# Kernel optimization log

Hardware: AMD Instinct MI355X
Metric: run time of the kernel (lower is better)

Reference implementation:

```python
import jax, jax.numpy as jnp
import numpy as np

N_NODES = 20000
N_EDGES = 320000
N_GRAPHS = 32
IN_CH = 5
HID = 64
HEADS = 4
DH = HID // HEADS  # 16
LAYERS = 8
EPS = 1e-5
SLOPE = 0.2


def setup_inputs() -> dict:
    key = jax.random.key(0)
    ks = jax.random.split(key, 32)
    inp = {}
    inp['x1'] = jax.random.normal(ks[0], (N_NODES, IN_CH), dtype=jnp.float32)
    inp['x2'] = jax.random.normal(ks[1], (N_NODES, IN_CH), dtype=jnp.float32)
    inp['edge_index1'] = jax.random.randint(ks[2], (2, N_EDGES), 0, N_NODES, dtype=jnp.int32)
    inp['edge_index2'] = jax.random.randint(ks[3], (2, N_EDGES), 0, N_NODES, dtype=jnp.int32)
    inp['batch1'] = jnp.sort(jax.random.randint(ks[4], (N_NODES,), 0, N_GRAPHS, dtype=jnp.int32))
    inp['batch2'] = jnp.sort(jax.random.randint(ks[5], (N_NODES,), 0, N_GRAPHS, dtype=jnp.int32))
    # node_lin
    inp['Wn'] = jax.random.normal(ks[6], (IN_CH, HID), dtype=jnp.float32) / np.sqrt(IN_CH)
    inp['bnode'] = jnp.zeros((HID,), dtype=jnp.float32)
    # GATv2 layers (stacked over LAYERS)
    s = 1.0 / np.sqrt(HID)
    inp['Wl'] = jax.random.normal(ks[7], (LAYERS, HID, HID), dtype=jnp.float32) * s
    inp['bl'] = jnp.zeros((LAYERS, HID), dtype=jnp.float32)
    inp['Wr'] = jax.random.normal(ks[8], (LAYERS, HID, HID), dtype=jnp.float32) * s
    inp['br'] = jnp.zeros((LAYERS, HID), dtype=jnp.float32)
    inp['att'] = jax.random.normal(ks[9], (LAYERS, HEADS, DH), dtype=jnp.float32) / np.sqrt(DH)
    inp['cbias'] = jnp.zeros((LAYERS, HID), dtype=jnp.float32)
    # batch norms
    inp['gamma'] = jnp.ones((LAYERS, HID), dtype=jnp.float32)
    inp['beta'] = jnp.zeros((LAYERS, HID), dtype=jnp.float32)
    # fc head
    inp['f1w'] = jax.random.normal(ks[10], (2 * HID, 256), dtype=jnp.float32) / np.sqrt(2 * HID)
    inp['f1b'] = jnp.zeros((256,), dtype=jnp.float32)
    inp['f2w'] = jax.random.normal(ks[11], (256, 128), dtype=jnp.float32) / np.sqrt(256)
    inp['f2b'] = jnp.zeros((128,), dtype=jnp.float32)
    inp['f3w'] = jax.random.normal(ks[12], (128, 1), dtype=jnp.float32) / np.sqrt(128)
    inp['f3b'] = jnp.zeros((1,), dtype=jnp.float32)
    return inp


def _gatv2_layer(x, src, dst, Wl, bl, Wr, br, att, bias):
    # x: [N, HID]; src/dst: [E'] (self loops included)
    N = x.shape[0]
    xl = (x @ Wl + bl).reshape(N, HEADS, DH)  # source transform
    xr = (x @ Wr + br).reshape(N, HEADS, DH)  # target transform
    e = jax.nn.leaky_relu(xl[src] + xr[dst], SLOPE)          # [E, H, DH]
    score = jnp.einsum('ehd,hd->eh', e, att)                  # [E, H]
    smax = jax.ops.segment_max(score, dst, num_segments=N)    # [N, H]
    ex = jnp.exp(score - smax[dst])
    denom = jax.ops.segment_sum(ex, dst, num_segments=N)
    alpha = ex / denom[dst]                                   # [E, H]
    msg = alpha[:, :, None] * xl[src]                         # [E, H, DH]
    out = jax.ops.segment_sum(msg, dst, num_segments=N)       # [N, H, DH]
    return out.reshape(N, HID) + bias


def _forward_once(x, edge_index, batch, Wn, bnode, Wl, bl, Wr, br, att, cbias, gamma, beta):
    N = x.shape[0]
    loop = jnp.arange(N, dtype=edge_index.dtype)
    src = jnp.concatenate([edge_index[0], loop])  # add_self_loops=True
    dst = jnp.concatenate([edge_index[1], loop])
    h = x @ Wn + bnode
    for l in range(LAYERS):
        g = _gatv2_layer(h, src, dst, Wl[l], bl[l], Wr[l], br[l], att[l], cbias[l])
        mu = g.mean(axis=0)
        var = g.var(axis=0)
        g = (g - mu) / jnp.sqrt(var + EPS) * gamma[l] + beta[l]
        h = h + jax.nn.elu(g)
    # global_mean_pool
    sums = jax.ops.segment_sum(h, batch, num_segments=N_GRAPHS)
    cnt = jax.ops.segment_sum(jnp.ones((N,), dtype=h.dtype), batch, num_segments=N_GRAPHS)
    return sums / jnp.maximum(cnt, 1.0)[:, None]


def reference(x1, edge_index1, batch1, x2, edge_index2, batch2, Wn, bnode, Wl, bl, Wr, br, att, cbias, gamma, beta, f1w, f1b, f2w, f2b, f3w, f3b):
    o1 = _forward_once(x1, edge_index1, batch1, Wn, bnode, Wl, bl, Wr, br, att, cbias, gamma, beta)
    o2 = _forward_once(x2, edge_index2, batch2, Wn, bnode, Wl, bl, Wr, br, att, cbias, gamma, beta)
    c = jnp.concatenate([o1, o2], axis=1)           # [G, 128]
    h = jax.nn.relu(c @ f1w + f1b)                   # dropout = identity (eval)
    h = jax.nn.relu(h @ f2w + f2b)
    return h @ f3w + f3b                             # [G, 1]
```

## Files before the change

### kernel.cpp

```cpp
#include <hip/hip_runtime.h>
#include <hip/hip_bf16.h>

#define N_NODES 20000
#define HID 64
#define EPS 1e-5f

struct GP {
    const int* ei;
    const int* batch;
    const float* x;
    int* deg;
    int* cursor;
    int* csr;
    float* h;
    float* xl;
    float* xr;
    float* gb;
    float* stats;
    float* osum;
};


__global__ void k_csr_init(GP a, GP b, int n, int two) {
    int t = blockIdx.x * blockDim.x + threadIdx.x;
    if (t < n) {
        a.deg[t] = 1;
        if (two) b.deg[t] = 1;
    }
}

__global__ void k_count(GP a, GP b, int Ea, int Eb, int two) {
    int t = blockIdx.x * blockDim.x + threadIdx.x;
    if (t < Ea) atomicAdd(&a.deg[a.ei[Ea + t]], 1);
    if (two && t < Eb) atomicAdd(&b.deg[b.ei[Eb + t]], 1);
}

#define SCAN_T 1024
#define SCAN_C 20
__global__ __launch_bounds__(1024) void k_scan(GP a, GP b, int n, int totA, int totB) {
    GP g = blockIdx.x ? b : a;
    int total = blockIdx.x ? totB : totA;
    __shared__ int sd[SCAN_T];
    int t = threadIdx.x;
    int base = t * SCAN_C;
    int loc[SCAN_C];
    int s = 0;
#pragma unroll
    for (int i = 0; i < SCAN_C; ++i) {
        int idx = base + i;
        loc[i] = (idx < n) ? g.deg[idx] : 0;
        s += loc[i];
    }
    sd[t] = s;
    __syncthreads();
    for (int off = 1; off < SCAN_T; off <<= 1) {
        int v = (t >= off) ? sd[t - off] : 0;
        __syncthreads();
        sd[t] += v;
        __syncthreads();
    }
    int run = sd[t] - s;
#pragma unroll
    for (int i = 0; i < SCAN_C; ++i) {
        int idx = base + i;
        if (idx < n) { g.deg[idx] = run; g.cursor[idx] = run; run += loc[i]; }
    }
    if (t == 0) g.deg[n] = total;
}

__global__ void k_scatter(GP a, GP b, int Ea, int Eb, int n, int two) {
    int t = blockIdx.x * blockDim.x + threadIdx.x;
    if (t < Ea) {
        int s = a.ei[t], d = a.ei[Ea + t];
        a.csr[atomicAdd(&a.cursor[d], 1)] = s;
    } else if (t < Ea + n) {
        int nn = t - Ea;
        a.csr[atomicAdd(&a.cursor[nn], 1)] = nn;
    }
    if (two) {
        if (t < Eb) {
            int s = b.ei[t], d = b.ei[Eb + t];
            b.csr[atomicAdd(&b.cursor[d], 1)] = s;
        } else if (t < Eb + n) {
            int nn = t - Eb;
            b.csr[atomicAdd(&b.cursor[nn], 1)] = nn;
        }
    }
}


__global__ void k_nodelin(GP a, GP b, int nPer, const float* __restrict__ Wn,
                          const float* __restrict__ bn, int n) {
    int bid = blockIdx.x;
    GP g = a;
    if (bid >= nPer) { g = b; bid -= nPer; }
    int idx = bid * 256 + threadIdx.x;
    if (idx >= n * HID) return;
    int node = idx >> 6, c = idx & 63;
    float acc = bn[c];
#pragma unroll
    for (int k = 0; k < 5; ++k) acc += g.x[node * 5 + k] * Wn[k * HID + c];
    g.h[idx] = acc;
}


__global__ __launch_bounds__(256) void k_lin2(GP ga, GP gbp, int nPer, int n,
        const float* __restrict__ Wl, const float* __restrict__ bl,
        const float* __restrict__ Wr, const float* __restrict__ br,
        const float* __restrict__ gamma, const float* __restrict__ beta, int layer) {
    __shared__ float wls[4096], wrs[4096];
    __shared__ float hs[2048];
    int bid = blockIdx.x;
    GP g = ga;
    if (bid >= nPer) { g = gbp; bid -= nPer; }
    {
        const float4* wl4 = (const float4*)Wl;
        const float4* wr4 = (const float4*)Wr;
        float4* l4 = (float4*)wls;
        float4* r4 = (float4*)wrs;
        for (int i = threadIdx.x; i < 1024; i += 256) { l4[i] = wl4[i]; r4[i] = wr4[i]; }
    }
    int c = threadIdx.x & 63;
    int wid = threadIdx.x >> 6;
    float blv = bl[c], brv = br[c];
    float mu = 0.f, inv = 1.f, gam = 1.f, bet = 0.f;
    if (layer > 0) {
        const float* st = g.stats + (layer - 1) * 128;
        float invn = 1.0f / (float)n;
        mu = st[c] * invn;
        float var = st[64 + c] * invn - mu * mu;
        inv = rsqrtf(fmaxf(var, 0.f) + EPS);
        gam = gamma[c]; bet = beta[c];
    }
    __syncthreads();
    float* hw = &hs[wid * 512];
    const float4* hw4 = (const float4*)hw;
    for (int base = bid * 32; base < n; base += nPer * 32) {
        int nb = base + wid * 8;
        size_t off0 = (size_t)nb * 64 + c;
        float hv[8];
        if (layer > 0) {
#pragma unroll
            for (int j = 0; j < 8; ++j) {
                float gv = g.gb[off0 + j * 64];
                float ov = g.h[off0 + j * 64];
                float v = (gv - mu) * inv * gam + bet;
                v = v > 0.f ? v : expm1f(v);
                hv[j] = ov + v;
                g.h[off0 + j * 64] = hv[j];
            }
        } else {
#pragma unroll
            for (int j = 0; j < 8; ++j) hv[j] = g.h[off0 + j * 64];
        }
#pragma unroll
        for (int j = 0; j < 8; ++j) hw[j * 64 + c] = hv[j];
        float accl[8], accr[8];
#pragma unroll
        for (int j = 0; j < 8; ++j) { accl[j] = blv; accr[j] = brv; }
        for (int k4 = 0; k4 < 16; ++k4) {
            float4 hq[8];
#pragma unroll
            for (int j = 0; j < 8; ++j) hq[j] = hw4[j * 16 + k4];
#pragma unroll
            for (int kk = 0; kk < 4; ++kk) {
                float wl = wls[(k4 * 4 + kk) * 64 + c];
                float wr = wrs[(k4 * 4 + kk) * 64 + c];
#pragma unroll
                for (int j = 0; j < 8; ++j) {
                    float hx = (&hq[j].x)[kk];
                    accl[j] = fmaf(hx, wl, accl[j]);
                    accr[j] = fmaf(hx, wr, accr[j]);
                }
            }
        }
#pragma unroll
        for (int j = 0; j < 8; ++j) {
            g.xl[off0 + j * 64] = accl[j];
            g.xr[off0 + j * 64] = accr[j];
        }
    }
}


__device__ __forceinline__ float red16(float p) {
    p += __int_as_float(__builtin_amdgcn_update_dpp(0, __float_as_int(p), 0xB1, 0xF, 0xF, true));
    p += __int_as_float(__builtin_amdgcn_update_dpp(0, __float_as_int(p), 0x4E, 0xF, 0xF, true));
    p += __int_as_float(__builtin_amdgcn_update_dpp(0, __float_as_int(p), 0x141, 0xF, 0xF, true));
    p += __int_as_float(__builtin_amdgcn_update_dpp(0, __float_as_int(p), 0x140, 0xF, 0xF, true));
    return p;
}

__global__ __launch_bounds__(512) void k_attn(GP ga, GP gbp, int nPer,
        const float* __restrict__ att, const float* __restrict__ cbias, int layer, int n) {
    int bid = blockIdx.x;
    GP g = ga;
    if (bid >= nPer) { g = gbp; bid -= nPer; }
    int lane = threadIdx.x & 63;
    int wid = threadIdx.x >> 6;
    int gw = bid * 8 + wid;
    int nw = nPer * 8;
    float attv = att[lane];
    float attv2 = attv * 0.2f;
    float cb = cbias[lane];
    const int* __restrict__ rowptr = g.deg;
    const int* __restrict__ csr = g.csr;
    const float* __restrict__ xl = g.xl;
    const float* __restrict__ xr = g.xr;
    float* __restrict__ gbuf = g.gb;
    float* st = g.stats + layer * 128;
    float bsum = 0.f, bsq = 0.f;
    for (int node = gw; node < n; node += nw) {
        int start = rowptr[node], end = rowptr[node + 1];
        float xrv = xr[(size_t)node * 64 + lane];
        float ts = xl[(size_t)node * 64 + lane] + xrv;
        float sself = red16(ts * (ts > 0.f ? attv : attv2));
        float lsum = 0.f, acc = 0.f;
        int idx = start;
        for (; idx + 8 <= end; idx += 8) {
            int sidx[8];
            float xv[8];
#pragma unroll
            for (int j = 0; j < 8; ++j) sidx[j] = csr[idx + j];
#pragma unroll
            for (int j = 0; j < 8; ++j) xv[j] = xl[(size_t)sidx[j] * 64 + lane];
#pragma unroll
            for (int j = 0; j < 8; ++j) {
                float t = xv[j] + xrv;
                float p = red16(t * (t > 0.f ? attv : attv2));
                float w = __expf(fminf(p - sself, 80.f));
                lsum += w;
                acc = fmaf(w, xv[j], acc);
            }
        }
        for (; idx + 4 <= end; idx += 4) {
            int sidx[4];
            float xv[4];
#pragma unroll
            for (int j = 0; j < 4; ++j) sidx[j] = csr[idx + j];
#pragma unroll
            for (int j = 0; j < 4; ++j) xv[j] = xl[(size_t)sidx[j] * 64 + lane];
#pragma unroll
            for (int j = 0; j < 4; ++j) {
                float t = xv[j] + xrv;
                float p = red16(t * (t > 0.f ? attv : attv2));
                float w = __expf(fminf(p - sself, 80.f));
                lsum += w;
                acc = fmaf(w, xv[j], acc);
            }
        }
        for (; idx < end; ++idx) {
            int s0 = csr[idx];
            float x0 = xl[(size_t)s0 * 64 + lane];
            float t0 = x0 + xrv;
            float p0 = red16(t0 * (t0 > 0.f ? attv : attv2));
            float w0 = __expf(fminf(p0 - sself, 80.f));
            lsum += w0;
            acc = fmaf(w0, x0, acc);
        }
        float outv = acc / lsum + cb;
        gbuf[(size_t)node * 64 + lane] = outv;
        bsum += outv; bsq += outv * outv;
    }
    __shared__ float sred[512];
    sred[threadIdx.x] = bsum;
    __syncthreads();
    if (threadIdx.x < 64) {
        float t = 0.f;
#pragma unroll
        for (int w = 0; w < 8; ++w) t += sred[w * 64 + threadIdx.x];
        atomicAdd(&st[threadIdx.x], t);
    }
    __syncthreads();
    sred[threadIdx.x] = bsq;
    __syncthreads();
    if (threadIdx.x < 64) {
        float t = 0.f;
#pragma unroll
        for (int w = 0; w < 8; ++w) t += sred[w * 64 + threadIdx.x];
        atomicAdd(&st[64 + threadIdx.x], t);
    }
}


__global__ __launch_bounds__(256) void k_pool(GP ga, GP gbp, int nPer,
        const float* __restrict__ gamma, const float* __restrict__ beta, int n) {
    int bid = blockIdx.x;
    GP g = ga;
    if (bid >= nPer) { g = gbp; bid -= nPer; }
    int lane = threadIdx.x & 63, w = threadIdx.x >> 6;
    const float* st = g.stats + 7 * 128;
    float invn = 1.f / (float)n;
    float mu = st[lane] * invn;
    float var = st[64 + lane] * invn - mu * mu;
    float inv = rsqrtf(fmaxf(var, 0.f) + EPS);
    float gam = gamma[lane], bet = beta[lane];
    int chunk = (n + nPer - 1) / nPer;
    int s = bid * chunk;
    int e = min(s + chunk, n);
    float acc = 0.f;
    int cur = -1;
    for (int node = s + w; node < e; node += 4) {
        int bg = g.batch[node];
        size_t off = (size_t)node * 64 + lane;
        float gv = g.gb[off];
        float hv = g.h[off];
        float v = (gv - mu) * inv * gam + bet;
        float hn = hv + (v > 0.f ? v : expm1f(v));
        if (bg != cur) {
            if (cur >= 0) atomicAdd(&g.osum[cur * 64 + lane], acc);
            acc = 0.f; cur = bg;
        }
        acc += hn;
    }
    if (cur >= 0) atomicAdd(&g.osum[cur * 64 + lane], acc);
}


__device__ __forceinline__ int lb(const int* __restrict__ b, int n, int v) {
    int lo = 0, hi = n;
    while (lo < hi) { int mid = (lo + hi) >> 1; if (b[mid] < v) lo = mid + 1; else hi = mid; }
    return lo;
}

__global__ __launch_bounds__(256) void k_fc(const float* __restrict__ o1, const float* __restrict__ o2,
                                            const int* __restrict__ b1, const int* __restrict__ b2,
                                            const float* __restrict__ f1w, const float* __restrict__ f1b,
                                            const float* __restrict__ f2w, const float* __restrict__ f2b,
                                            const float* __restrict__ f3w, const float* __restrict__ f3b,
                                            float* __restrict__ out, int n) {
    int gid = blockIdx.x, t = threadIdx.x;
    __shared__ float cin[128];
    __shared__ float h1[256];
    __shared__ float red[128];
    __shared__ int cnts[2];
    if (t == 0) cnts[0] = lb(b1, n, gid + 1) - lb(b1, n, gid);
    if (t == 1) cnts[1] = lb(b2, n, gid + 1) - lb(b2, n, gid);
    __syncthreads();
    if (t < 64) {
        float c1 = (float)(cnts[0] > 0 ? cnts[0] : 1);
        float c2 = (float)(cnts[1] > 0 ? cnts[1] : 1);
        cin[t] = o1[gid * 64 + t] / c1;
        cin[64 + t] = o2[gid * 64 + t] / c2;
    }
    __syncthreads();
    float a = f1b[t];
#pragma unroll 8
    for (int k = 0; k < 128; ++k) a += cin[k] * f1w[k * 256 + t];
    h1[t] = fmaxf(a, 0.f);
    __syncthreads();
    if (t < 128) {
        float a2 = f2b[t];
#pragma unroll 8
        for (int k = 0; k < 256; ++k) a2 += h1[k] * f2w[k * 128 + t];
        red[t] = fmaxf(a2, 0.f) * f3w[t];
    }
    __syncthreads();
    for (int off = 64; off > 0; off >>= 1) {
        if (t < off) red[t] += red[t + off];
        __syncthreads();
    }
    if (t == 0) out[gid] = red[0] + f3b[0];
}


extern "C" void kernel_launch(void* const* d_in, const int* in_sizes, int n_in,
                              void* d_out, int out_size, void* d_ws, size_t ws_size,
                              hipStream_t stream) {
    const float* x1 = (const float*)d_in[0];
    const float* x2 = (const float*)d_in[1];
    const int* ei1 = (const int*)d_in[2];
    const int* ei2 = (const int*)d_in[3];
    const int* b1 = (const int*)d_in[4];
    const int* b2 = (const int*)d_in[5];
    const float* Wn = (const float*)d_in[6];
    const float* bnode = (const float*)d_in[7];
    const float* Wl = (const float*)d_in[8];
    const float* bl = (const float*)d_in[9];
    const float* Wr = (const float*)d_in[10];
    const float* br = (const float*)d_in[11];
    const float* att = (const float*)d_in[12];
    const float* cbias = (const float*)d_in[13];
    const float* gamma = (const float*)d_in[14];
    const float* beta = (const float*)d_in[15];
    const float* f1w = (const float*)d_in[16];
    const float* f1b = (const float*)d_in[17];
    const float* f2w = (const float*)d_in[18];
    const float* f2b = (const float*)d_in[19];
    const float* f3w = (const float*)d_in[20];
    const float* f3b = (const float*)d_in[21];
    float* out = (float*)d_out;

    const int N = N_NODES;
    const int EA = in_sizes[2] / 2;
    const int EB = in_sizes[3] / 2;
    const size_t INT_PG = 20096 + 20096 + 340096;
    const size_t BIG = (size_t)N * 64;
    const size_t SMALL = 2 * 1024 + 2 * 2048;
    const size_t dualBytes = 2 * INT_PG * 4 + (8 * BIG + SMALL) * 4;
    const int dual = (ws_size >= dualBytes) ? 1 : 0;

    int* ibase = (int*)d_ws;
    int* iA = ibase;
    int* iB = dual ? ibase + INT_PG : ibase;
    float* fbase = (float*)(ibase + (size_t)(dual ? 2 : 1) * INT_PG);
    float* hA = fbase;
    float* xlA = hA + BIG;
    float* xrA = xlA + BIG;
    float* gbA = xrA + BIG;
    float* hB = dual ? gbA + BIG : hA;
    float* xlB = dual ? hB + BIG : xlA;
    float* xrB = dual ? xlB + BIG : xrA;
    float* gbB = dual ? xrB + BIG : gbA;
    float* small = dual ? gbB + BIG : gbA + BIG;
    float* statsA = small;
    float* statsB = small + 1024;
    float* osumA = small + 2048;
    float* osumB = small + 4096;

    GP A, B;
    A.ei = ei1; A.batch = b1; A.x = x1;
    A.deg = iA; A.cursor = iA + 20096; A.csr = iA + 40192;
    A.h = hA; A.xl = xlA; A.xr = xrA; A.gb = gbA; A.stats = statsA; A.osum = osumA;
    B.ei = ei2; B.batch = b2; B.x = x2;
    B.deg = iB; B.cursor = iB + 20096; B.csr = iB + 40192;
    B.h = hB; B.xl = xlB; B.xr = xrB; B.gb = gbB; B.stats = statsB; B.osum = osumB;

    hipMemsetAsync(small, 0, SMALL * sizeof(float), stream);

    const int LIN2_NB = 320;
    const int ATT_NB = 512;
    const int POOL_NB = 250;

    if (dual) {
        int Emax = EA > EB ? EA : EB;
        k_csr_init<<<(N + 255) / 256, 256, 0, stream>>>(A, B, N, 1);
        k_count<<<(Emax + 255) / 256, 256, 0, stream>>>(A, B, EA, EB, 1);
        k_scan<<<2, 1024, 0, stream>>>(A, B, N, EA + N, EB + N);
        k_scatter<<<(Emax + N + 255) / 256, 256, 0, stream>>>(A, B, EA, EB, N, 1);
        k_nodelin<<<2 * ((N * 64) / 256), 256, 0, stream>>>(A, B, (N * 64) / 256, Wn, bnode, N);
        for (int l = 0; l < 8; ++l) {
            const float* gm = l ? gamma + (l - 1) * 64 : gamma;
            const float* bt = l ? beta + (l - 1) * 64 : beta;
            k_lin2<<<2 * LIN2_NB, 256, 0, stream>>>(A, B, LIN2_NB, N, Wl + l * 4096, bl + l * 64,
                                                    Wr + l * 4096, br + l * 64, gm, bt, l);
            k_attn<<<2 * ATT_NB, 512, 0, stream>>>(A, B, ATT_NB, att + l * 64, cbias + l * 64, l, N);
        }
        k_pool<<<2 * POOL_NB, 256, 0, stream>>>(A, B, POOL_NB, gamma + 7 * 64, beta + 7 * 64, N);
    } else {
        for (int gi = 0; gi < 2; ++gi) {
            GP G = gi ? B : A;
            int E = gi ? EB : EA;
            k_csr_init<<<(N + 255) / 256, 256, 0, stream>>>(G, G, N, 0);
            k_count<<<(E + 255) / 256, 256, 0, stream>>>(G, G, E, E, 0);
            k_scan<<<1, 1024, 0, stream>>>(G, G, N, E + N, E + N);
            k_scatter<<<(E + N + 255) / 256, 256, 0, stream>>>(G, G, E, E, N, 0);
            k_nodelin<<<(N * 64) / 256, 256, 0, stream>>>(G, G, (N * 64) / 256, Wn, bnode, N);
            for (int l = 0; l < 8; ++l) {
                const float* gm = l ? gamma + (l - 1) * 64 : gamma;
                const float* bt = l ? beta + (l - 1) * 64 : beta;
                k_lin2<<<LIN2_NB, 256, 0, stream>>>(G, G, LIN2_NB, N, Wl + l * 4096, bl + l * 64,
                                                    Wr + l * 4096, br + l * 64, gm, bt, l);
                k_attn<<<ATT_NB, 512, 0, stream>>>(G, G, ATT_NB, att + l * 64, cbias + l * 64, l, N);
            }
            k_pool<<<POOL_NB, 256, 0, stream>>>(G, G, POOL_NB, gamma + 7 * 64, beta + 7 * 64, N);
        }
    }
    k_fc<<<32, 256, 0, stream>>>(osumA, osumB, b1, b2, f1w, f1b, f2w, f2b, f3w, f3b, out, N);
}
```

Measured before the change: 754.1 us.

## Store source features in fp16 and widen attention blocks to 1024 threads

The source-transformed features xl are now written as half precision by the linear kernel and read as half in the attention gather, halving the bytes moved by the random per-edge neighbor loads. The attention kernel now runs 16 waves per block with graph selection interleaved by block parity, and it uses nontemporal loads for CSR indices and xr and a nontemporal store for its output. The fp16 storage lowers accuracy of the attention logits and aggregation. In the non-dual path the launch now covers both halves with the same GP, so half the blocks repeat the work of the other half.

Measured after the change: 780.0 us. 1.03x slower.

```diff
diff --git a/kernel.cpp b/kernel.cpp
--- a/kernel.cpp
+++ b/kernel.cpp
@@ -1,5 +1,6 @@
 #include <hip/hip_runtime.h>
 #include <hip/hip_bf16.h>
+#include <hip/hip_fp16.h>
 
 #define N_NODES 20000
 #define HID 64
@@ -13,7 +14,7 @@
     int* cursor;
     int* csr;
     float* h;
-    float* xl;
+    __half* xlh;
     float* xr;
     float* gb;
     float* stats;
@@ -176,7 +177,7 @@
         }
 #pragma unroll
         for (int j = 0; j < 8; ++j) {
-            g.xl[off0 + j * 64] = accl[j];
+            g.xlh[off0 + j * 64] = __float2half(accl[j]);
             g.xr[off0 + j * 64] = accr[j];
         }
     }
@@ -191,29 +192,30 @@
     return p;
 }
 
-__global__ __launch_bounds__(512) void k_attn(GP ga, GP gbp, int nPer,
+__global__ __launch_bounds__(1024) void k_attn(GP ga, GP gbp, int nPer,
         const float* __restrict__ att, const float* __restrict__ cbias, int layer, int n) {
     int bid = blockIdx.x;
-    GP g = ga;
-    if (bid >= nPer) { g = gbp; bid -= nPer; }
+    GP g = (bid & 1) ? gbp : ga;
+    bid >>= 1;
     int lane = threadIdx.x & 63;
     int wid = threadIdx.x >> 6;
-    int gw = bid * 8 + wid;
-    int nw = nPer * 8;
+    int gw = bid * 16 + wid;
+    int nw = nPer * 16;
     float attv = att[lane];
     float attv2 = attv * 0.2f;
     float cb = cbias[lane];
     const int* __restrict__ rowptr = g.deg;
     const int* __restrict__ csr = g.csr;
-    const float* __restrict__ xl = g.xl;
+    const __half* __restrict__ xl = g.xlh;
     const float* __restrict__ xr = g.xr;
     float* __restrict__ gbuf = g.gb;
     float* st = g.stats + layer * 128;
     float bsum = 0.f, bsq = 0.f;
     for (int node = gw; node < n; node += nw) {
         int start = rowptr[node], end = rowptr[node + 1];
-        float xrv = xr[(size_t)node * 64 + lane];
-        float ts = xl[(size_t)node * 64 + lane] + xrv;
+        float xrv = __builtin_nontemporal_load(&xr[(size_t)node * 64 + lane]);
+        float xself = __half2float(xl[(size_t)node * 64 + lane]);
+        float ts = xself + xrv;
         float sself = red16(ts * (ts > 0.f ? attv : attv2));
         float lsum = 0.f, acc = 0.f;
         int idx = start;
@@ -221,9 +223,9 @@
             int sidx[8];
             float xv[8];
 #pragma unroll
-            for (int j = 0; j < 8; ++j) sidx[j] = csr[idx + j];
-#pragma unroll
-            for (int j = 0; j < 8; ++j) xv[j] = xl[(size_t)sidx[j] * 64 + lane];
+            for (int j = 0; j < 8; ++j) sidx[j] = __builtin_nontemporal_load(&csr[idx + j]);
+#pragma unroll
+            for (int j = 0; j < 8; ++j) xv[j] = __half2float(xl[(size_t)sidx[j] * 64 + lane]);
 #pragma unroll
             for (int j = 0; j < 8; ++j) {
                 float t = xv[j] + xrv;
@@ -237,9 +239,9 @@
             int sidx[4];
             float xv[4];
 #pragma unroll
-            for (int j = 0; j < 4; ++j) sidx[j] = csr[idx + j];
-#pragma unroll
-            for (int j = 0; j < 4; ++j) xv[j] = xl[(size_t)sidx[j] * 64 + lane];
+            for (int j = 0; j < 4; ++j) sidx[j] = __builtin_nontemporal_load(&csr[idx + j]);
+#pragma unroll
+            for (int j = 0; j < 4; ++j) xv[j] = __half2float(xl[(size_t)sidx[j] * 64 + lane]);
 #pragma unroll
             for (int j = 0; j < 4; ++j) {
                 float t = xv[j] + xrv;
@@ -250,8 +252,8 @@
             }
         }
         for (; idx < end; ++idx) {
-            int s0 = csr[idx];
-            float x0 = xl[(size_t)s0 * 64 + lane];
+            int s0 = __builtin_nontemporal_load(&csr[idx]);
+            float x0 = __half2float(xl[(size_t)s0 * 64 + lane]);
             float t0 = x0 + xrv;
             float p0 = red16(t0 * (t0 > 0.f ? attv : attv2));
             float w0 = __expf(fminf(p0 - sself, 80.f));
@@ -259,16 +261,16 @@
             acc = fmaf(w0, x0, acc);
         }
         float outv = acc / lsum + cb;
-        gbuf[(size_t)node * 64 + lane] = outv;
+        __builtin_nontemporal_store(outv, &gbuf[(size_t)node * 64 + lane]);
         bsum += outv; bsq += outv * outv;
     }
-    __shared__ float sred[512];
+    __shared__ float sred[1024];
     sred[threadIdx.x] = bsum;
     __syncthreads();
     if (threadIdx.x < 64) {
         float t = 0.f;
 #pragma unroll
-        for (int w = 0; w < 8; ++w) t += sred[w * 64 + threadIdx.x];
+        for (int w = 0; w < 16; ++w) t += sred[w * 64 + threadIdx.x];
         atomicAdd(&st[threadIdx.x], t);
     }
     __syncthreads();
@@ -277,7 +279,7 @@
     if (threadIdx.x < 64) {
         float t = 0.f;
 #pragma unroll
-        for (int w = 0; w < 8; ++w) t += sred[w * 64 + threadIdx.x];
+        for (int w = 0; w < 16; ++w) t += sred[w * 64 + threadIdx.x];
         atomicAdd(&st[64 + threadIdx.x], t);
     }
 }
@@ -421,15 +423,15 @@
     GP A, B;
     A.ei = ei1; A.batch = b1; A.x = x1;
     A.deg = iA; A.cursor = iA + 20096; A.csr = iA + 40192;
-    A.h = hA; A.xl = xlA; A.xr = xrA; A.gb = gbA; A.stats = statsA; A.osum = osumA;
+    A.h = hA; A.xlh = (__half*)xlA; A.xr = xrA; A.gb = gbA; A.stats = statsA; A.osum = osumA;
     B.ei = ei2; B.batch = b2; B.x = x2;
     B.deg = iB; B.cursor = iB + 20096; B.csr = iB + 40192;
-    B.h = hB; B.xl = xlB; B.xr = xrB; B.gb = gbB; B.stats = statsB; B.osum = osumB;
+    B.h = hB; B.xlh = (__half*)xlB; B.xr = xrB; B.gb = gbB; B.stats = statsB; B.osum = osumB;
 
     hipMemsetAsync(small, 0, SMALL * sizeof(float), stream);
 
     const int LIN2_NB = 320;
-    const int ATT_NB = 512;
+    const int ATT_NB = 256;
     const int POOL_NB = 250;
 
     if (dual) {
@@ -444,7 +446,7 @@
             const float* bt = l ? beta + (l - 1) * 64 : beta;
             k_lin2<<<2 * LIN2_NB, 256, 0, stream>>>(A, B, LIN2_NB, N, Wl + l * 4096, bl + l * 64,
                                                     Wr + l * 4096, br + l * 64, gm, bt, l);
-            k_attn<<<2 * ATT_NB, 512, 0, stream>>>(A, B, ATT_NB, att + l * 64, cbias + l * 64, l, N);
+            k_attn<<<2 * ATT_NB, 1024, 0, stream>>>(A, B, ATT_NB, att + l * 64, cbias + l * 64, l, N);
         }
         k_pool<<<2 * POOL_NB, 256, 0, stream>>>(A, B, POOL_NB, gamma + 7 * 64, beta + 7 * 64, N);
     } else {
@@ -461,7 +463,7 @@
                 const float* bt = l ? beta + (l - 1) * 64 : beta;
                 k_lin2<<<LIN2_NB, 256, 0, stream>>>(G, G, LIN2_NB, N, Wl + l * 4096, bl + l * 64,
                                                     Wr + l * 4096, br + l * 64, gm, bt, l);
-                k_attn<<<ATT_NB, 512, 0, stream>>>(G, G, ATT_NB, att + l * 64, cbias + l * 64, l, N);
+                k_attn<<<2 * ATT_NB, 1024, 0, stream>>>(G, G, ATT_NB, att + l * 64, cbias + l * 64, l, N);
             }
             k_pool<<<POOL_NB, 256, 0, stream>>>(G, G, POOL_NB, gamma + 7 * 64, beta + 7 * 64, N);
         }
```
